# Optimization experiments

Measured on AMD Instinct MI355X. Metric: run time of the kernel, lower is better.

The kernel has to match this reference:

```python
import jax, jax.numpy as jnp
import numpy as np

N_EMBD = 1024
N_HEAD = 16

def setup_inputs() -> dict:
    key = jax.random.key(0)
    ks = jax.random.split(key, 5)
    B, T, C = 4, 2048, N_EMBD
    scale = 1.0 / np.sqrt(C)
    return {
        "x": jax.random.normal(ks[0], (B, T, C), dtype=jnp.float32),
        "w_qkv": jax.random.normal(ks[1], (C, 3 * C), dtype=jnp.float32) * scale,
        "b_qkv": jax.random.normal(ks[2], (3 * C,), dtype=jnp.float32) * 0.02,
        "w_proj": jax.random.normal(ks[3], (C, C), dtype=jnp.float32) * scale,
        "b_proj": jax.random.normal(ks[4], (C,), dtype=jnp.float32) * 0.02,
    }

def reference(x, w_qkv, b_qkv, w_proj, b_proj):
    B, T, C = x.shape
    H = N_HEAD
    D = C // H  # head dim
    qkv = x @ w_qkv + b_qkv  # [B,T,3C]
    q, k, v = jnp.split(qkv, 3, axis=-1)
    # [B,T,C] -> [B,H,T,D]
    q = q.reshape(B, T, H, D).transpose(0, 2, 1, 3)
    k = k.reshape(B, T, H, D).transpose(0, 2, 1, 3)
    v = v.reshape(B, T, H, D).transpose(0, 2, 1, 3)
    att = jnp.einsum("bhqd,bhkd->bhqk", q, k) / jnp.sqrt(jnp.asarray(D, x.dtype))
    causal = jnp.tril(jnp.ones((T, T), dtype=bool))  # [T,T]
    att = jnp.where(causal[None, None, :, :], att, -jnp.inf)
    att = jax.nn.softmax(att, axis=-1)
    y = jnp.einsum("bhqk,bhkd->bhqd", att, v)  # [B,H,T,D]
    y = y.transpose(0, 2, 1, 3).reshape(B, T, C)
    return y @ w_proj + b_proj
```

## Files before the change

### kernel.cpp

```cpp
#include <hip/hip_runtime.h>
#include <hip/hip_bf16.h>
#include <stdint.h>

typedef __bf16 bf16_8 __attribute__((ext_vector_type(8)));
typedef float f32_4 __attribute__((ext_vector_type(4)));
typedef short short4v __attribute__((ext_vector_type(4)));

static __device__ __forceinline__ unsigned short f2bf(float f) {
    union { float f; unsigned int u; } v; v.f = f;
    unsigned int u = v.u;
    unsigned int r = (u + 0x7fffu + ((u >> 16) & 1u)) >> 16;
    return (unsigned short)r;
}

static __device__ __forceinline__ unsigned int pack_bf16x2(float a, float b) {
    union { float f; unsigned int u; } ua, ub;
    ua.f = a; ub.f = b;
    return __builtin_amdgcn_perm(ub.u + 0x8000u, ua.u + 0x8000u, 0x07060302u);
}

static __device__ __forceinline__ f32_4 mfma_16x16x16_bf16(short4v a, short4v b, f32_4 c) {
#if __has_builtin(__builtin_amdgcn_mfma_f32_16x16x16bf16_1k)
    return __builtin_amdgcn_mfma_f32_16x16x16bf16_1k(a, b, c, 0, 0, 0);
#else
    asm volatile("v_mfma_f32_16x16x16_bf16 %0, %1, %2, %0"
                 : "+v"(c) : "v"(a), "v"(b));
    return c;
#endif
}

static __device__ __forceinline__ void gll16(const unsigned short* g, unsigned short* l) {
    __builtin_amdgcn_global_load_lds(
        (const __attribute__((address_space(1))) unsigned int*)g,
        (__attribute__((address_space(3))) unsigned int*)l, 16, 0, 0);
}

__global__ __launch_bounds__(256) void prep_kernel(
    const float* __restrict__ x, unsigned int* __restrict__ xbf,
    const float* __restrict__ w_qkv, unsigned short* __restrict__ wqkvt,
    const float* __restrict__ w_proj, unsigned short* __restrict__ wprojt) {
    __shared__ unsigned short tile[64][65];
    int bid = blockIdx.x;
    if (bid < 8192) {
        int i = bid * 256 + threadIdx.x;
        float4 f = ((const float4*)x)[i];
        uint2 o;
        o.x = pack_bf16x2(f.x, f.y);
        o.y = pack_bf16x2(f.z, f.w);
        ((uint2*)xbf)[i] = o;
        return;
    }
    const float* in; unsigned short* out; int N, bx, by;
    if (bid < 8960) {
        in = w_qkv; out = wqkvt; N = 3072;
        int t = bid - 8192; bx = t % 48; by = t / 48;
    } else {
        in = w_proj; out = wprojt; N = 1024;
        int t = bid - 8960; bx = t & 15; by = t >> 4;
    }
    const int K = 1024;
    int k0 = by * 64, n0 = bx * 64;
    int tc = threadIdx.x & 63, tr = threadIdx.x >> 6;
    for (int p = 0; p < 16; ++p) {
        int k = p * 4 + tr;
        tile[k][tc] = f2bf(in[(size_t)(k0 + k) * N + n0 + tc]);
    }
    __syncthreads();
    for (int p = 0; p < 16; ++p) {
        int n = p * 4 + tr;
        out[(size_t)(n0 + n) * K + k0 + tc] = tile[tc][n];
    }
}

#define BK 64
#define QSCALE 0.1803368801111204f

__global__ __launch_bounds__(256) void gemm_qkv(
    const unsigned short* __restrict__ A,
    const unsigned short* __restrict__ Bt,
    const float* __restrict__ bias,
    int M, int N, int K,
    unsigned short* __restrict__ q_out, unsigned short* __restrict__ k_out,
    unsigned short* __restrict__ v_out) {
    __shared__ __align__(16) unsigned short As[128 * BK];
    __shared__ __align__(16) unsigned short Bs[128 * BK];
    int tid = threadIdx.x;
    int wave = tid >> 6, lane = tid & 63;
    int wm = wave & 1, wn = wave >> 1;
    int quad = lane >> 4, l16 = lane & 15;
    int m0 = blockIdx.y * 128, n0 = blockIdx.x * 128;
    int which = n0 >> 10;

    f32_4 acc[4][4] = {};

    int srow = lane >> 3;
    int scs = ((lane & 7) ^ srow) * 8;
    const unsigned short* Ag = A + (size_t)(m0 + wave * 32 + srow) * K + scs;
    const unsigned short* Bg = Bt + (size_t)(n0 + wave * 32 + srow) * K + scs;
    unsigned short* Asl = As + wave * 32 * BK;
    unsigned short* Bsl = Bs + wave * 32 * BK;
    int sx = l16 & 7;

    for (int kt = 0; kt < K; kt += BK) {
        for (int p = 0; p < 4; ++p) {
            gll16(Ag + kt + (size_t)(8 * p) * K, Asl + p * 8 * BK);
            gll16(Bg + kt + (size_t)(8 * p) * K, Bsl + p * 8 * BK);
        }
        __syncthreads();
        bf16_8 af[4][2], bfr[4][2];
        for (int i = 0; i < 4; ++i)
            for (int ks = 0; ks < 2; ++ks)
                af[i][ks] = *(const bf16_8*)(As + (wm * 64 + i * 16 + l16) * BK +
                                             ((unsigned)((ks * 4 + quad) ^ sx)) * 8);
        for (int j = 0; j < 4; ++j)
            for (int ks = 0; ks < 2; ++ks)
                bfr[j][ks] = *(const bf16_8*)(Bs + (wn * 64 + j * 16 + l16) * BK +
                                              ((unsigned)((ks * 4 + quad) ^ sx)) * 8);
        if (which < 2) {
            for (int i = 0; i < 4; ++i)
                for (int j = 0; j < 4; ++j) {
                    acc[i][j] = __builtin_amdgcn_mfma_f32_16x16x32_bf16(bfr[j][0], af[i][0], acc[i][j], 0, 0, 0);
                    acc[i][j] = __builtin_amdgcn_mfma_f32_16x16x32_bf16(bfr[j][1], af[i][1], acc[i][j], 0, 0, 0);
                }
        } else {
            for (int i = 0; i < 4; ++i)
                for (int j = 0; j < 4; ++j) {
                    acc[i][j] = __builtin_amdgcn_mfma_f32_16x16x32_bf16(af[i][0], bfr[j][0], acc[i][j], 0, 0, 0);
                    acc[i][j] = __builtin_amdgcn_mfma_f32_16x16x32_bf16(af[i][1], bfr[j][1], acc[i][j], 0, 0, 0);
                }
        }
        __syncthreads();
    }

    int b = m0 >> 11;
    int tbase = (m0 & 2047) + wm * 64;
    int nw0 = n0 + wn * 64;
    if (which < 2) {
        unsigned short* dst = which == 0 ? q_out : k_out;
        float scale = which == 0 ? QSCALE : 1.0f;
        int h0 = ((n0 & 1023) >> 6) + wn;
        size_t base = ((size_t)((b << 4) + h0) * 2048) * 64;
        for (int j = 0; j < 4; ++j) {
            float4 b4 = *(const float4*)(bias + nw0 + j * 16 + quad * 4);
            int d0 = j * 16 + quad * 4;
            for (int i = 0; i < 4; ++i) {
                int t = tbase + i * 16 + l16;
                uint2 pk;
                pk.x = pack_bf16x2((acc[i][j][0] + b4.x) * scale,
                                   (acc[i][j][1] + b4.y) * scale);
                pk.y = pack_bf16x2((acc[i][j][2] + b4.z) * scale,
                                   (acc[i][j][3] + b4.w) * scale);
                *(uint2*)(dst + base + (size_t)t * 64 + d0) = pk;
            }
        }
    } else {
        for (int j = 0; j < 4; ++j) {
            int n = nw0 + j * 16 + l16;
            int c = n & 1023, h = c >> 6, d = c & 63;
            float bs = bias[n];
            size_t base = ((size_t)((b << 4) + h) * 64 + d) * 2048;
            for (int i = 0; i < 4; ++i) {
                int t0 = tbase + i * 16 + quad * 4;
                uint2 pk;
                pk.x = pack_bf16x2(acc[i][j][0] + bs, acc[i][j][1] + bs);
                pk.y = pack_bf16x2(acc[i][j][2] + bs, acc[i][j][3] + bs);
                *(uint2*)(v_out + base + t0) = pk;
            }
        }
    }
}

__global__ __launch_bounds__(256) void gemm_proj(
    const unsigned short* __restrict__ A,
    const unsigned short* __restrict__ Bt,
    const float* __restrict__ bias,
    int M, int N, int K, float* __restrict__ outf) {
    __shared__ __align__(16) unsigned short As[128 * BK];
    __shared__ __align__(16) unsigned short Bs[128 * BK];
    int tid = threadIdx.x;
    int wave = tid >> 6, lane = tid & 63;
    int wm = wave & 1, wn = wave >> 1;
    int quad = lane >> 4, l16 = lane & 15;
    int m0 = blockIdx.y * 128, n0 = blockIdx.x * 128;

    f32_4 acc[4][4] = {};

    int srow = lane >> 3;
    int scs = ((lane & 7) ^ srow) * 8;
    const unsigned short* Ag = A + (size_t)(m0 + wave * 32 + srow) * K + scs;
    const unsigned short* Bg = Bt + (size_t)(n0 + wave * 32 + srow) * K + scs;
    unsigned short* Asl = As + wave * 32 * BK;
    unsigned short* Bsl = Bs + wave * 32 * BK;
    int sx = l16 & 7;

    for (int kt = 0; kt < K; kt += BK) {
        for (int p = 0; p < 4; ++p) {
            gll16(Ag + kt + (size_t)(8 * p) * K, Asl + p * 8 * BK);
            gll16(Bg + kt + (size_t)(8 * p) * K, Bsl + p * 8 * BK);
        }
        __syncthreads();
        bf16_8 af[4][2], bfr[4][2];
        for (int i = 0; i < 4; ++i)
            for (int ks = 0; ks < 2; ++ks)
                af[i][ks] = *(const bf16_8*)(As + (wm * 64 + i * 16 + l16) * BK +
                                             ((unsigned)((ks * 4 + quad) ^ sx)) * 8);
        for (int j = 0; j < 4; ++j)
            for (int ks = 0; ks < 2; ++ks)
                bfr[j][ks] = *(const bf16_8*)(Bs + (wn * 64 + j * 16 + l16) * BK +
                                              ((unsigned)((ks * 4 + quad) ^ sx)) * 8);
        for (int i = 0; i < 4; ++i)
            for (int j = 0; j < 4; ++j) {
                acc[i][j] = __builtin_amdgcn_mfma_f32_16x16x32_bf16(af[i][0], bfr[j][0], acc[i][j], 0, 0, 0);
                acc[i][j] = __builtin_amdgcn_mfma_f32_16x16x32_bf16(af[i][1], bfr[j][1], acc[i][j], 0, 0, 0);
            }
        __syncthreads();
    }

    for (int j = 0; j < 4; ++j) {
        int n = n0 + wn * 64 + j * 16 + l16;
        float bs = bias[n];
        for (int i = 0; i < 4; ++i) {
            int m = m0 + wm * 64 + i * 16 + quad * 4;
            for (int r = 0; r < 4; ++r)
                outf[(size_t)(m + r) * N + n] = acc[i][j][r] + bs;
        }
    }
}

__global__ __launch_bounds__(256, 5) void attn_kernel(
    const unsigned short* __restrict__ Q, const unsigned short* __restrict__ Kb,
    const unsigned short* __restrict__ Vt, unsigned short* __restrict__ Y,
    int T) {
    __shared__ __align__(16) unsigned short KsB[2][64 * 64];
    __shared__ __align__(16) unsigned short VtsB[2][64 * 64];

    int tid = threadIdx.x;
    int wave = tid >> 6, lane = tid & 63;
    int quad = lane >> 4, l16 = lane & 15;
    int bh = blockIdx.x;
    int b = bh >> 4, h = bh & 15;
    int qt = 31 - blockIdx.y;
    int qw = qt * 64 + wave * 16;
    int nkt = qt + 1;

    int srow = lane >> 3;
    int scs = ((lane & 7) ^ srow) * 8;
    int sx = l16 & 7;

    bf16_8 qa[2];
    for (int ks = 0; ks < 2; ++ks)
        qa[ks] = *(const bf16_8*)(Q + ((size_t)bh * T + qw + l16) * 64 + ks * 32 + quad * 8);

    f32_4 o[4] = {};
    f32_4 osum = {};
    short4v vones;
    { unsigned short one = 0x3F80;
      vones[0] = (short)one; vones[1] = (short)one; vones[2] = (short)one; vones[3] = (short)one; }

    for (int p = 0; p < 2; ++p) {
        int row = wave * 16 + p * 8;
        gll16(Kb + ((size_t)bh * T + row + srow) * 64 + scs, &KsB[0][row * 64]);
        gll16(Vt + ((size_t)bh * 64 + row + srow) * (size_t)T + scs, &VtsB[0][row * 64]);
    }
    __syncthreads();

    for (int kt = 0; kt < nkt; ++kt) {
        int cur = kt & 1;
        int kb = kt * 64;
        if (kt + 1 < nkt) {
            int kb2 = kb + 64, nxt = cur ^ 1;
            for (int p = 0; p < 2; ++p) {
                int row = wave * 16 + p * 8;
                gll16(Kb + ((size_t)bh * T + kb2 + row + srow) * 64 + scs, &KsB[nxt][row * 64]);
                gll16(Vt + ((size_t)bh * 64 + row + srow) * (size_t)T + kb2 + scs, &VtsB[nxt][row * 64]);
            }
        }
        const unsigned short* KsC = KsB[cur];
        const unsigned short* VtsC = VtsB[cur];

        f32_4 s[4] = {};
        for (int kf = 0; kf < 4; ++kf) {
            bf16_8 k0 = *(const bf16_8*)(KsC + (kf * 16 + l16) * 64 + ((unsigned)(quad ^ sx)) * 8);
            bf16_8 k1 = *(const bf16_8*)(KsC + (kf * 16 + l16) * 64 + ((unsigned)((4 + quad) ^ sx)) * 8);
            s[kf] = __builtin_amdgcn_mfma_f32_16x16x32_bf16(k0, qa[0], s[kf], 0, 0, 0);
            s[kf] = __builtin_amdgcn_mfma_f32_16x16x32_bf16(k1, qa[1], s[kf], 0, 0, 0);
        }

        if (kt == qt) {
            int q = qw + l16;
            for (int kf = 0; kf < 4; ++kf) {
                int kk = kb + kf * 16 + quad * 4;
                for (int r = 0; r < 4; ++r)
                    if (kk + r > q) s[kf][r] = -1e30f;
            }
        }

        short4v pb[4];
        for (int kf = 0; kf < 4; ++kf) {
            float p0 = __builtin_amdgcn_exp2f(s[kf][0]);
            float p1 = __builtin_amdgcn_exp2f(s[kf][1]);
            float p2 = __builtin_amdgcn_exp2f(s[kf][2]);
            float p3 = __builtin_amdgcn_exp2f(s[kf][3]);
            union { unsigned int u[2]; short4v s4; } pu;
            pu.u[0] = pack_bf16x2(p0, p1);
            pu.u[1] = pack_bf16x2(p2, p3);
            pb[kf] = pu.s4;
        }

        for (int kf = 0; kf < 4; ++kf) {
            osum = mfma_16x16x16_bf16(vones, pb[kf], osum);
            unsigned voff = ((unsigned)((2 * kf + (quad >> 1)) ^ sx)) * 8 + (quad & 1) * 4;
            for (int df = 0; df < 4; ++df) {
                short4v va = *(const short4v*)(VtsC + (df * 16 + l16) * 64 + voff);
                o[df] = mfma_16x16x16_bf16(va, pb[kf], o[df]);
            }
        }
        __syncthreads();
    }

    float inv = 1.0f / osum[0];
    unsigned short* yp = Y + ((size_t)b * T + qw + l16) * 1024 + h * 64 + quad * 4;
    for (int df = 0; df < 4; ++df) {
        uint2 pk;
        pk.x = pack_bf16x2(o[df][0] * inv, o[df][1] * inv);
        pk.y = pack_bf16x2(o[df][2] * inv, o[df][3] * inv);
        *(uint2*)(yp + df * 16) = pk;
    }
}

extern "C" void kernel_launch(void* const* d_in, const int* in_sizes, int n_in,
                              void* d_out, int out_size, void* d_ws, size_t ws_size,
                              hipStream_t stream) {
    const float* x = (const float*)d_in[0];
    const float* w_qkv = (const float*)d_in[1];
    const float* b_qkv = (const float*)d_in[2];
    const float* w_proj = (const float*)d_in[3];
    const float* b_proj = (const float*)d_in[4];
    float* out = (float*)d_out;

    unsigned short* xbf = (unsigned short*)d_ws;
    unsigned short* wqkvt = xbf + 8388608;
    unsigned short* wprojt = wqkvt + 3145728;
    unsigned short* Qb = wprojt + 1048576;
    unsigned short* Kb = Qb + 8388608;
    unsigned short* Vtb = Kb + 8388608;
    unsigned short* Yb = Vtb + 8388608;

    hipLaunchKernelGGL(prep_kernel, dim3(9216), dim3(256), 0, stream,
                       x, (unsigned int*)xbf, w_qkv, wqkvt, w_proj, wprojt);
    hipLaunchKernelGGL(gemm_qkv, dim3(24, 64), dim3(256), 0, stream,
                       xbf, wqkvt, b_qkv, 8192, 3072, 1024,
                       Qb, Kb, Vtb);
    hipLaunchKernelGGL(attn_kernel, dim3(64, 32), dim3(256), 0, stream,
                       Qb, Kb, Vtb, Yb, 2048);
    hipLaunchKernelGGL(gemm_proj, dim3(8, 64), dim3(256), 0, stream,
                       Yb, wprojt, b_proj, 8192, 1024, 1024, out);
}
```

Measured before the change: 256.7 us.

## Restructure QKV GEMM into 256x128 tiles with triple-buffered async LDS pipeline

Measured after the change: 666.9 us. 2.6x slower.

```diff
diff --git a/kernel.cpp b/kernel.cpp
--- a/kernel.cpp
+++ b/kernel.cpp
@@ -5,6 +5,8 @@
 typedef __bf16 bf16_8 __attribute__((ext_vector_type(8)));
 typedef float f32_4 __attribute__((ext_vector_type(4)));
 typedef short short4v __attribute__((ext_vector_type(4)));
+
+#define VMCNT(n) asm volatile("s_waitcnt vmcnt(" #n ")" ::: "memory")
 
 static __device__ __forceinline__ unsigned short f2bf(float f) {
     union { float f; unsigned int u; } v; v.f = f;
@@ -75,65 +77,96 @@
 #define BK 64
 #define QSCALE 0.1803368801111204f
 
-__global__ __launch_bounds__(256) void gemm_qkv(
+__global__ __launch_bounds__(256, 2) void gemm_qkv(
     const unsigned short* __restrict__ A,
     const unsigned short* __restrict__ Bt,
     const float* __restrict__ bias,
     int M, int N, int K,
     unsigned short* __restrict__ q_out, unsigned short* __restrict__ k_out,
     unsigned short* __restrict__ v_out) {
-    __shared__ __align__(16) unsigned short As[128 * BK];
-    __shared__ __align__(16) unsigned short Bs[128 * BK];
+    __shared__ __align__(16) unsigned short Ash[3][256 * 32];
+    __shared__ __align__(16) unsigned short Bsh[3][128 * 32];
     int tid = threadIdx.x;
     int wave = tid >> 6, lane = tid & 63;
-    int wm = wave & 1, wn = wave >> 1;
     int quad = lane >> 4, l16 = lane & 15;
-    int m0 = blockIdx.y * 128, n0 = blockIdx.x * 128;
+    int wm = wave >> 1, wn = wave & 1;
+
+    int bid = blockIdx.x;
+    int flat = (bid & 7) * 96 + (bid >> 3);
+    int bm = flat / 24, bn = flat - bm * 24;
+    int m0 = bm * 256, n0 = bn * 128;
     int which = n0 >> 10;
 
-    f32_4 acc[4][4] = {};
-
-    int srow = lane >> 3;
-    int scs = ((lane & 7) ^ srow) * 8;
-    const unsigned short* Ag = A + (size_t)(m0 + wave * 32 + srow) * K + scs;
-    const unsigned short* Bg = Bt + (size_t)(n0 + wave * 32 + srow) * K + scs;
-    unsigned short* Asl = As + wave * 32 * BK;
-    unsigned short* Bsl = Bs + wave * 32 * BK;
-    int sx = l16 & 7;
-
-    for (int kt = 0; kt < K; kt += BK) {
-        for (int p = 0; p < 4; ++p) {
-            gll16(Ag + kt + (size_t)(8 * p) * K, Asl + p * 8 * BK);
-            gll16(Bg + kt + (size_t)(8 * p) * K, Bsl + p * 8 * BK);
-        }
-        __syncthreads();
-        bf16_8 af[4][2], bfr[4][2];
+    f32_4 acc[8][4] = {};
+
+    int srow = lane >> 2;
+    int gch = ((lane & 3) ^ (srow & 3)) * 8;
+    const unsigned short* Ag = A + (size_t)(m0 + wave * 16 + srow) * K + gch;
+    const unsigned short* Bg = Bt + (size_t)(n0 + wave * 16 + srow) * K + gch;
+
+    unsigned short *pa0 = Ash[0], *pa1 = Ash[1], *pa2 = Ash[2];
+    unsigned short *pb0 = Bsh[0], *pb1 = Bsh[1], *pb2 = Bsh[2];
+
+    int ktiles = K >> 5;
+    int sx8 = (quad ^ (l16 & 3)) * 8;
+
+#define STAGE_QKV(Ad, Bd, kc) do { \
+        for (int p = 0; p < 4; ++p) \
+            gll16(Ag + (kc) + (size_t)(p * 64) * K, (Ad) + (p * 64 + wave * 16) * 32); \
+        for (int p = 0; p < 2; ++p) \
+            gll16(Bg + (kc) + (size_t)(p * 64) * K, (Bd) + (p * 64 + wave * 16) * 32); \
+    } while (0)
+
+    STAGE_QKV(pa0, pb0, 0);
+    STAGE_QKV(pa1, pb1, 32);
+    VMCNT(6);
+    __builtin_amdgcn_s_barrier();
+
+    for (int kt = 0; kt < ktiles; ++kt) {
+        if (kt + 2 < ktiles) {
+            int kc = (kt + 2) << 5;
+            STAGE_QKV(pa2, pb2, kc);
+        }
+        __builtin_amdgcn_sched_barrier(0);
+
+        bf16_8 af[4], ag2[4], bfr[4];
         for (int i = 0; i < 4; ++i)
-            for (int ks = 0; ks < 2; ++ks)
-                af[i][ks] = *(const bf16_8*)(As + (wm * 64 + i * 16 + l16) * BK +
-                                             ((unsigned)((ks * 4 + quad) ^ sx)) * 8);
+            af[i] = *(const bf16_8*)(pa0 + (wm * 128 + i * 16 + l16) * 32 + sx8);
         for (int j = 0; j < 4; ++j)
-            for (int ks = 0; ks < 2; ++ks)
-                bfr[j][ks] = *(const bf16_8*)(Bs + (wn * 64 + j * 16 + l16) * BK +
-                                              ((unsigned)((ks * 4 + quad) ^ sx)) * 8);
+            bfr[j] = *(const bf16_8*)(pb0 + (wn * 64 + j * 16 + l16) * 32 + sx8);
+        for (int i = 0; i < 4; ++i)
+            ag2[i] = *(const bf16_8*)(pa0 + (wm * 128 + (i + 4) * 16 + l16) * 32 + sx8);
+
+        __builtin_amdgcn_s_setprio(1);
         if (which < 2) {
             for (int i = 0; i < 4; ++i)
-                for (int j = 0; j < 4; ++j) {
-                    acc[i][j] = __builtin_amdgcn_mfma_f32_16x16x32_bf16(bfr[j][0], af[i][0], acc[i][j], 0, 0, 0);
-                    acc[i][j] = __builtin_amdgcn_mfma_f32_16x16x32_bf16(bfr[j][1], af[i][1], acc[i][j], 0, 0, 0);
-                }
+                for (int j = 0; j < 4; ++j)
+                    acc[i][j] = __builtin_amdgcn_mfma_f32_16x16x32_bf16(bfr[j], af[i], acc[i][j], 0, 0, 0);
+            for (int i = 0; i < 4; ++i)
+                for (int j = 0; j < 4; ++j)
+                    acc[i + 4][j] = __builtin_amdgcn_mfma_f32_16x16x32_bf16(bfr[j], ag2[i], acc[i + 4][j], 0, 0, 0);
         } else {
             for (int i = 0; i < 4; ++i)
-                for (int j = 0; j < 4; ++j) {
-                    acc[i][j] = __builtin_amdgcn_mfma_f32_16x16x32_bf16(af[i][0], bfr[j][0], acc[i][j], 0, 0, 0);
-                    acc[i][j] = __builtin_amdgcn_mfma_f32_16x16x32_bf16(af[i][1], bfr[j][1], acc[i][j], 0, 0, 0);
-                }
-        }
-        __syncthreads();
-    }
+                for (int j = 0; j < 4; ++j)
+                    acc[i][j] = __builtin_amdgcn_mfma_f32_16x16x32_bf16(af[i], bfr[j], acc[i][j], 0, 0, 0);
+            for (int i = 0; i < 4; ++i)
+                for (int j = 0; j < 4; ++j)
+                    acc[i + 4][j] = __builtin_amdgcn_mfma_f32_16x16x32_bf16(ag2[i], bfr[j], acc[i + 4][j], 0, 0, 0);
+        }
+        __builtin_amdgcn_s_setprio(0);
+
+        if (kt + 1 < ktiles) {
+            if (kt + 2 < ktiles) { VMCNT(6); } else { VMCNT(0); }
+            __builtin_amdgcn_s_barrier();
+        }
+        unsigned short* t;
+        t = pa0; pa0 = pa1; pa1 = pa2; pa2 = t;
+        t = pb0; pb0 = pb1; pb1 = pb2; pb2 = t;
+    }
+#undef STAGE_QKV
 
     int b = m0 >> 11;
-    int tbase = (m0 & 2047) + wm * 64;
+    int tbase = (m0 & 2047) + wm * 128;
     int nw0 = n0 + wn * 64;
     if (which < 2) {
         unsigned short* dst = which == 0 ? q_out : k_out;
@@ -143,7 +176,7 @@
         for (int j = 0; j < 4; ++j) {
             float4 b4 = *(const float4*)(bias + nw0 + j * 16 + quad * 4);
             int d0 = j * 16 + quad * 4;
-            for (int i = 0; i < 4; ++i) {
+            for (int i = 0; i < 8; ++i) {
                 int t = tbase + i * 16 + l16;
                 uint2 pk;
                 pk.x = pack_bf16x2((acc[i][j][0] + b4.x) * scale,
@@ -159,7 +192,7 @@
             int c = n & 1023, h = c >> 6, d = c & 63;
             float bs = bias[n];
             size_t base = ((size_t)((b << 4) + h) * 64 + d) * 2048;
-            for (int i = 0; i < 4; ++i) {
+            for (int i = 0; i < 8; ++i) {
                 int t0 = tbase + i * 16 + quad * 4;
                 uint2 pk;
                 pk.x = pack_bf16x2(acc[i][j][0] + bs, acc[i][j][1] + bs);
@@ -348,7 +381,7 @@
 
     hipLaunchKernelGGL(prep_kernel, dim3(9216), dim3(256), 0, stream,
                        x, (unsigned int*)xbf, w_qkv, wqkvt, w_proj, wprojt);
-    hipLaunchKernelGGL(gemm_qkv, dim3(24, 64), dim3(256), 0, stream,
+    hipLaunchKernelGGL(gemm_qkv, dim3(768), dim3(256), 0, stream,
                        xbf, wqkvt, b_qkv, 8192, 3072, 1024,
                        Qb, Kb, Vtb);
     hipLaunchKernelGGL(attn_kernel, dim3(64, 32), dim3(256), 0, stream,
```

## Double-buffer LDS tiles in QKV and projection GEMMs to overlap loads

Applied to the files above, without the earlier changes.

Measured after the change: 254.5 us. About the same (-0.9%).

```diff
diff --git a/kernel.cpp b/kernel.cpp
--- a/kernel.cpp
+++ b/kernel.cpp
@@ -82,8 +82,8 @@
     int M, int N, int K,
     unsigned short* __restrict__ q_out, unsigned short* __restrict__ k_out,
     unsigned short* __restrict__ v_out) {
-    __shared__ __align__(16) unsigned short As[128 * BK];
-    __shared__ __align__(16) unsigned short Bs[128 * BK];
+    __shared__ __align__(16) unsigned short As[2][128 * BK];
+    __shared__ __align__(16) unsigned short Bs[2][128 * BK];
     int tid = threadIdx.x;
     int wave = tid >> 6, lane = tid & 63;
     int wm = wave & 1, wn = wave >> 1;
@@ -97,24 +97,34 @@
     int scs = ((lane & 7) ^ srow) * 8;
     const unsigned short* Ag = A + (size_t)(m0 + wave * 32 + srow) * K + scs;
     const unsigned short* Bg = Bt + (size_t)(n0 + wave * 32 + srow) * K + scs;
-    unsigned short* Asl = As + wave * 32 * BK;
-    unsigned short* Bsl = Bs + wave * 32 * BK;
+    int sbase = wave * 32 * BK;
     int sx = l16 & 7;
 
+    for (int p = 0; p < 4; ++p) {
+        gll16(Ag + (size_t)(8 * p) * K, As[0] + sbase + p * 8 * BK);
+        gll16(Bg + (size_t)(8 * p) * K, Bs[0] + sbase + p * 8 * BK);
+    }
+    __syncthreads();
+
+    int cur = 0;
     for (int kt = 0; kt < K; kt += BK) {
-        for (int p = 0; p < 4; ++p) {
-            gll16(Ag + kt + (size_t)(8 * p) * K, Asl + p * 8 * BK);
-            gll16(Bg + kt + (size_t)(8 * p) * K, Bsl + p * 8 * BK);
-        }
-        __syncthreads();
+        if (kt + BK < K) {
+            int nxt = cur ^ 1;
+            for (int p = 0; p < 4; ++p) {
+                gll16(Ag + kt + BK + (size_t)(8 * p) * K, As[nxt] + sbase + p * 8 * BK);
+                gll16(Bg + kt + BK + (size_t)(8 * p) * K, Bs[nxt] + sbase + p * 8 * BK);
+            }
+        }
+        const unsigned short* Ac = As[cur];
+        const unsigned short* Bc = Bs[cur];
         bf16_8 af[4][2], bfr[4][2];
         for (int i = 0; i < 4; ++i)
             for (int ks = 0; ks < 2; ++ks)
-                af[i][ks] = *(const bf16_8*)(As + (wm * 64 + i * 16 + l16) * BK +
+                af[i][ks] = *(const bf16_8*)(Ac + (wm * 64 + i * 16 + l16) * BK +
                                              ((unsigned)((ks * 4 + quad) ^ sx)) * 8);
         for (int j = 0; j < 4; ++j)
             for (int ks = 0; ks < 2; ++ks)
-                bfr[j][ks] = *(const bf16_8*)(Bs + (wn * 64 + j * 16 + l16) * BK +
+                bfr[j][ks] = *(const bf16_8*)(Bc + (wn * 64 + j * 16 + l16) * BK +
                                               ((unsigned)((ks * 4 + quad) ^ sx)) * 8);
         if (which < 2) {
             for (int i = 0; i < 4; ++i)
@@ -130,6 +140,7 @@
                 }
         }
         __syncthreads();
+        cur ^= 1;
     }
 
     int b = m0 >> 11;
@@ -175,8 +186,8 @@
     const unsigned short* __restrict__ Bt,
     const float* __restrict__ bias,
     int M, int N, int K, float* __restrict__ outf) {
-    __shared__ __align__(16) unsigned short As[128 * BK];
-    __shared__ __align__(16) unsigned short Bs[128 * BK];
+    __shared__ __align__(16) unsigned short As[2][128 * BK];
+    __shared__ __align__(16) unsigned short Bs[2][128 * BK];
     int tid = threadIdx.x;
     int wave = tid >> 6, lane = tid & 63;
     int wm = wave & 1, wn = wave >> 1;
@@ -189,24 +200,34 @@
     int scs = ((lane & 7) ^ srow) * 8;
     const unsigned short* Ag = A + (size_t)(m0 + wave * 32 + srow) * K + scs;
     const unsigned short* Bg = Bt + (size_t)(n0 + wave * 32 + srow) * K + scs;
-    unsigned short* Asl = As + wave * 32 * BK;
-    unsigned short* Bsl = Bs + wave * 32 * BK;
+    int sbase = wave * 32 * BK;
     int sx = l16 & 7;
 
+    for (int p = 0; p < 4; ++p) {
+        gll16(Ag + (size_t)(8 * p) * K, As[0] + sbase + p * 8 * BK);
+        gll16(Bg + (size_t)(8 * p) * K, Bs[0] + sbase + p * 8 * BK);
+    }
+    __syncthreads();
+
+    int cur = 0;
     for (int kt = 0; kt < K; kt += BK) {
-        for (int p = 0; p < 4; ++p) {
-            gll16(Ag + kt + (size_t)(8 * p) * K, Asl + p * 8 * BK);
-            gll16(Bg + kt + (size_t)(8 * p) * K, Bsl + p * 8 * BK);
-        }
-        __syncthreads();
+        if (kt + BK < K) {
+            int nxt = cur ^ 1;
+            for (int p = 0; p < 4; ++p) {
+                gll16(Ag + kt + BK + (size_t)(8 * p) * K, As[nxt] + sbase + p * 8 * BK);
+                gll16(Bg + kt + BK + (size_t)(8 * p) * K, Bs[nxt] + sbase + p * 8 * BK);
+            }
+        }
+        const unsigned short* Ac = As[cur];
+        const unsigned short* Bc = Bs[cur];
         bf16_8 af[4][2], bfr[4][2];
         for (int i = 0; i < 4; ++i)
             for (int ks = 0; ks < 2; ++ks)
-                af[i][ks] = *(const bf16_8*)(As + (wm * 64 + i * 16 + l16) * BK +
+                af[i][ks] = *(const bf16_8*)(Ac + (wm * 64 + i * 16 + l16) * BK +
                                              ((unsigned)((ks * 4 + quad) ^ sx)) * 8);
         for (int j = 0; j < 4; ++j)
             for (int ks = 0; ks < 2; ++ks)
-                bfr[j][ks] = *(const bf16_8*)(Bs + (wn * 64 + j * 16 + l16) * BK +
+                bfr[j][ks] = *(const bf16_8*)(Bc + (wn * 64 + j * 16 + l16) * BK +
                                               ((unsigned)((ks * 4 + quad) ^ sx)) * 8);
         for (int i = 0; i < 4; ++i)
             for (int j = 0; j < 4; ++j) {
@@ -214,6 +235,7 @@
                 acc[i][j] = __builtin_amdgcn_mfma_f32_16x16x32_bf16(af[i][1], bfr[j][1], acc[i][j], 0, 0, 0);
             }
         __syncthreads();
+        cur ^= 1;
     }
 
     for (int j = 0; j < 4; ++j) {
```

## Triple-buffer GEMM tiles with async prefetch and 256x128 block tiles

Applied to the files above, without the earlier changes.

After: 262.1 us. +2.1%, slower.

```diff
diff --git a/kernel.cpp b/kernel.cpp
--- a/kernel.cpp
+++ b/kernel.cpp
@@ -5,6 +5,11 @@
 typedef __bf16 bf16_8 __attribute__((ext_vector_type(8)));
 typedef float f32_4 __attribute__((ext_vector_type(4)));
 typedef short short4v __attribute__((ext_vector_type(4)));
+
+#define VMCNT(n) asm volatile("s_waitcnt vmcnt(" #n ")" ::: "memory")
+#define LGKM0 asm volatile("s_waitcnt lgkmcnt(0)" ::: "memory")
+#define SBAR __builtin_amdgcn_s_barrier()
+#define SCHB __builtin_amdgcn_sched_barrier(0)
 
 static __device__ __forceinline__ unsigned short f2bf(float f) {
     union { float f; unsigned int u; } v; v.f = f;
@@ -72,23 +77,22 @@
     }
 }
 
-#define BK 64
 #define QSCALE 0.1803368801111204f
 
-__global__ __launch_bounds__(256) void gemm_qkv(
+__global__ __launch_bounds__(512) void gemm_qkv(
     const unsigned short* __restrict__ A,
     const unsigned short* __restrict__ Bt,
     const float* __restrict__ bias,
     int M, int N, int K,
     unsigned short* __restrict__ q_out, unsigned short* __restrict__ k_out,
     unsigned short* __restrict__ v_out) {
-    __shared__ __align__(16) unsigned short As[128 * BK];
-    __shared__ __align__(16) unsigned short Bs[128 * BK];
+    __shared__ __align__(16) unsigned short As[3][256 * 64];
+    __shared__ __align__(16) unsigned short Bs[3][128 * 64];
     int tid = threadIdx.x;
     int wave = tid >> 6, lane = tid & 63;
-    int wm = wave & 1, wn = wave >> 1;
+    int wm = wave >> 1, wn = wave & 1;
     int quad = lane >> 4, l16 = lane & 15;
-    int m0 = blockIdx.y * 128, n0 = blockIdx.x * 128;
+    int m0 = blockIdx.y * 256, n0 = blockIdx.x * 128;
     int which = n0 >> 10;
 
     f32_4 acc[4][4] = {};
@@ -96,41 +100,78 @@
     int srow = lane >> 3;
     int scs = ((lane & 7) ^ srow) * 8;
     const unsigned short* Ag = A + (size_t)(m0 + wave * 32 + srow) * K + scs;
-    const unsigned short* Bg = Bt + (size_t)(n0 + wave * 32 + srow) * K + scs;
-    unsigned short* Asl = As + wave * 32 * BK;
-    unsigned short* Bsl = Bs + wave * 32 * BK;
+    const unsigned short* Bg = Bt + (size_t)(n0 + wave * 16 + srow) * K + scs;
     int sx = l16 & 7;
 
-    for (int kt = 0; kt < K; kt += BK) {
-        for (int p = 0; p < 4; ++p) {
-            gll16(Ag + kt + (size_t)(8 * p) * K, Asl + p * 8 * BK);
-            gll16(Bg + kt + (size_t)(8 * p) * K, Bsl + p * 8 * BK);
-        }
-        __syncthreads();
-        bf16_8 af[4][2], bfr[4][2];
-        for (int i = 0; i < 4; ++i)
-            for (int ks = 0; ks < 2; ++ks)
-                af[i][ks] = *(const bf16_8*)(As + (wm * 64 + i * 16 + l16) * BK +
-                                             ((unsigned)((ks * 4 + quad) ^ sx)) * 8);
+    unsigned short *a0 = As[0], *a1 = As[1], *a2 = As[2];
+    unsigned short *b0 = Bs[0], *b1 = Bs[1], *b2 = Bs[2];
+
+#define STG_A(dst, kc) do { \
+        for (int g = 0; g < 4; ++g) \
+            gll16(Ag + (kc) + (size_t)(g * 8) * K, (dst) + (wave * 32 + g * 8) * 64); \
+    } while (0)
+#define STG_B(dst, kc) do { \
+        for (int g = 0; g < 2; ++g) \
+            gll16(Bg + (kc) + (size_t)(g * 8) * K, (dst) + (wave * 16 + g * 8) * 64); \
+    } while (0)
+
+    STG_A(a0, 0); STG_B(b0, 0);
+    STG_A(a1, 64); STG_B(b1, 64);
+
+    const int nkt = K >> 6;
+    for (int kt = 0; kt < nkt; ++kt) {
+        if (kt + 1 < nkt) { VMCNT(6); } else { VMCNT(0); }
+        SCHB; SBAR; SCHB;
+        bf16_8 af[4], bfr[4];
+        for (int i = 0; i < 4; ++i)
+            af[i] = *(const bf16_8*)(a0 + (wm * 64 + i * 16 + l16) * 64 +
+                                     ((unsigned)(quad ^ sx)) * 8);
         for (int j = 0; j < 4; ++j)
-            for (int ks = 0; ks < 2; ++ks)
-                bfr[j][ks] = *(const bf16_8*)(Bs + (wn * 64 + j * 16 + l16) * BK +
-                                              ((unsigned)((ks * 4 + quad) ^ sx)) * 8);
+            bfr[j] = *(const bf16_8*)(b0 + (wn * 64 + j * 16 + l16) * 64 +
+                                      ((unsigned)(quad ^ sx)) * 8);
+        if (kt + 2 < nkt) STG_A(a2, (kt + 2) * 64);
+        SCHB; SBAR; SCHB;
+        LGKM0; SCHB;
+        __builtin_amdgcn_s_setprio(1);
         if (which < 2) {
             for (int i = 0; i < 4; ++i)
-                for (int j = 0; j < 4; ++j) {
-                    acc[i][j] = __builtin_amdgcn_mfma_f32_16x16x32_bf16(bfr[j][0], af[i][0], acc[i][j], 0, 0, 0);
-                    acc[i][j] = __builtin_amdgcn_mfma_f32_16x16x32_bf16(bfr[j][1], af[i][1], acc[i][j], 0, 0, 0);
-                }
+                for (int j = 0; j < 4; ++j)
+                    acc[i][j] = __builtin_amdgcn_mfma_f32_16x16x32_bf16(bfr[j], af[i], acc[i][j], 0, 0, 0);
         } else {
             for (int i = 0; i < 4; ++i)
-                for (int j = 0; j < 4; ++j) {
-                    acc[i][j] = __builtin_amdgcn_mfma_f32_16x16x32_bf16(af[i][0], bfr[j][0], acc[i][j], 0, 0, 0);
-                    acc[i][j] = __builtin_amdgcn_mfma_f32_16x16x32_bf16(af[i][1], bfr[j][1], acc[i][j], 0, 0, 0);
-                }
-        }
-        __syncthreads();
-    }
+                for (int j = 0; j < 4; ++j)
+                    acc[i][j] = __builtin_amdgcn_mfma_f32_16x16x32_bf16(af[i], bfr[j], acc[i][j], 0, 0, 0);
+        }
+        __builtin_amdgcn_s_setprio(0);
+
+        SCHB; SBAR; SCHB;
+        for (int i = 0; i < 4; ++i)
+            af[i] = *(const bf16_8*)(a0 + (wm * 64 + i * 16 + l16) * 64 +
+                                     ((unsigned)((4 + quad) ^ sx)) * 8);
+        for (int j = 0; j < 4; ++j)
+            bfr[j] = *(const bf16_8*)(b0 + (wn * 64 + j * 16 + l16) * 64 +
+                                      ((unsigned)((4 + quad) ^ sx)) * 8);
+        if (kt + 2 < nkt) STG_B(b2, (kt + 2) * 64);
+        SCHB; SBAR; SCHB;
+        LGKM0; SCHB;
+        __builtin_amdgcn_s_setprio(1);
+        if (which < 2) {
+            for (int i = 0; i < 4; ++i)
+                for (int j = 0; j < 4; ++j)
+                    acc[i][j] = __builtin_amdgcn_mfma_f32_16x16x32_bf16(bfr[j], af[i], acc[i][j], 0, 0, 0);
+        } else {
+            for (int i = 0; i < 4; ++i)
+                for (int j = 0; j < 4; ++j)
+                    acc[i][j] = __builtin_amdgcn_mfma_f32_16x16x32_bf16(af[i], bfr[j], acc[i][j], 0, 0, 0);
+        }
+        __builtin_amdgcn_s_setprio(0);
+
+        unsigned short* t;
+        t = a0; a0 = a1; a1 = a2; a2 = t;
+        t = b0; b0 = b1; b1 = b2; b2 = t;
+    }
+#undef STG_A
+#undef STG_B
 
     int b = m0 >> 11;
     int tbase = (m0 & 2047) + wm * 64;
@@ -170,51 +211,84 @@
     }
 }
 
-__global__ __launch_bounds__(256) void gemm_proj(
+__global__ __launch_bounds__(512) void gemm_proj(
     const unsigned short* __restrict__ A,
     const unsigned short* __restrict__ Bt,
     const float* __restrict__ bias,
     int M, int N, int K, float* __restrict__ outf) {
-    __shared__ __align__(16) unsigned short As[128 * BK];
-    __shared__ __align__(16) unsigned short Bs[128 * BK];
+    __shared__ __align__(16) unsigned short As[3][256 * 64];
+    __shared__ __align__(16) unsigned short Bs[3][128 * 64];
     int tid = threadIdx.x;
     int wave = tid >> 6, lane = tid & 63;
-    int wm = wave & 1, wn = wave >> 1;
+    int wm = wave >> 1, wn = wave & 1;
     int quad = lane >> 4, l16 = lane & 15;
-    int m0 = blockIdx.y * 128, n0 = blockIdx.x * 128;
+    int m0 = blockIdx.y * 256, n0 = blockIdx.x * 128;
 
     f32_4 acc[4][4] = {};
 
     int srow = lane >> 3;
     int scs = ((lane & 7) ^ srow) * 8;
     const unsigned short* Ag = A + (size_t)(m0 + wave * 32 + srow) * K + scs;
-    const unsigned short* Bg = Bt + (size_t)(n0 + wave * 32 + srow) * K + scs;
-    unsigned short* Asl = As + wave * 32 * BK;
-    unsigned short* Bsl = Bs + wave * 32 * BK;
+    const unsigned short* Bg = Bt + (size_t)(n0 + wave * 16 + srow) * K + scs;
     int sx = l16 & 7;
 
-    for (int kt = 0; kt < K; kt += BK) {
-        for (int p = 0; p < 4; ++p) {
-            gll16(Ag + kt + (size_t)(8 * p) * K, Asl + p * 8 * BK);
-            gll16(Bg + kt + (size_t)(8 * p) * K, Bsl + p * 8 * BK);
-        }
-        __syncthreads();
-        bf16_8 af[4][2], bfr[4][2];
-        for (int i = 0; i < 4; ++i)
-            for (int ks = 0; ks < 2; ++ks)
-                af[i][ks] = *(const bf16_8*)(As + (wm * 64 + i * 16 + l16) * BK +
-                                             ((unsigned)((ks * 4 + quad) ^ sx)) * 8);
+    unsigned short *a0 = As[0], *a1 = As[1], *a2 = As[2];
+    unsigned short *b0 = Bs[0], *b1 = Bs[1], *b2 = Bs[2];
+
+#define STG_A(dst, kc) do { \
+        for (int g = 0; g < 4; ++g) \
+            gll16(Ag + (kc) + (size_t)(g * 8) * K, (dst) + (wave * 32 + g * 8) * 64); \
+    } while (0)
+#define STG_B(dst, kc) do { \
+        for (int g = 0; g < 2; ++g) \
+            gll16(Bg + (kc) + (size_t)(g * 8) * K, (dst) + (wave * 16 + g * 8) * 64); \
+    } while (0)
+
+    STG_A(a0, 0); STG_B(b0, 0);
+    STG_A(a1, 64); STG_B(b1, 64);
+
+    const int nkt = K >> 6;
+    for (int kt = 0; kt < nkt; ++kt) {
+        if (kt + 1 < nkt) { VMCNT(6); } else { VMCNT(0); }
+        SCHB; SBAR; SCHB;
+        bf16_8 af[4], bfr[4];
+        for (int i = 0; i < 4; ++i)
+            af[i] = *(const bf16_8*)(a0 + (wm * 64 + i * 16 + l16) * 64 +
+                                     ((unsigned)(quad ^ sx)) * 8);
         for (int j = 0; j < 4; ++j)
-            for (int ks = 0; ks < 2; ++ks)
-                bfr[j][ks] = *(const bf16_8*)(Bs + (wn * 64 + j * 16 + l16) * BK +
-                                              ((unsigned)((ks * 4 + quad) ^ sx)) * 8);
-        for (int i = 0; i < 4; ++i)
-            for (int j = 0; j < 4; ++j) {
-                acc[i][j] = __builtin_amdgcn_mfma_f32_16x16x32_bf16(af[i][0], bfr[j][0], acc[i][j], 0, 0, 0);
-                acc[i][j] = __builtin_amdgcn_mfma_f32_16x16x32_bf16(af[i][1], bfr[j][1], acc[i][j], 0, 0, 0);
-            }
-        __syncthreads();
-    }
+            bfr[j] = *(const bf16_8*)(b0 + (wn * 64 + j * 16 + l16) * 64 +
+                                      ((unsigned)(quad ^ sx)) * 8);
+        if (kt + 2 < nkt) STG_A(a2, (kt + 2) * 64);
+        SCHB; SBAR; SCHB;
+        LGKM0; SCHB;
+        __builtin_amdgcn_s_setprio(1);
+        for (int i = 0; i < 4; ++i)
+            for (int j = 0; j < 4; ++j)
+                acc[i][j] = __builtin_amdgcn_mfma_f32_16x16x32_bf16(af[i], bfr[j], acc[i][j], 0, 0, 0);
+        __builtin_amdgcn_s_setprio(0);
+
+        SCHB; SBAR; SCHB;
+        for (int i = 0; i < 4; ++i)
+            af[i] = *(const bf16_8*)(a0 + (wm * 64 + i * 16 + l16) * 64 +
+                                     ((unsigned)((4 + quad) ^ sx)) * 8);
+        for (int j = 0; j < 4; ++j)
+            bfr[j] = *(const bf16_8*)(b0 + (wn * 64 + j * 16 + l16) * 64 +
+                                      ((unsigned)((4 + quad) ^ sx)) * 8);
+        if (kt + 2 < nkt) STG_B(b2, (kt + 2) * 64);
+        SCHB; SBAR; SCHB;
+        LGKM0; SCHB;
+        __builtin_amdgcn_s_setprio(1);
+        for (int i = 0; i < 4; ++i)
+            for (int j = 0; j < 4; ++j)
+                acc[i][j] = __builtin_amdgcn_mfma_f32_16x16x32_bf16(af[i], bfr[j], acc[i][j], 0, 0, 0);
+        __builtin_amdgcn_s_setprio(0);
+
+        unsigned short* t;
+        t = a0; a0 = a1; a1 = a2; a2 = t;
+        t = b0; b0 = b1; b1 = b2; b2 = t;
+    }
+#undef STG_A
+#undef STG_B
 
     for (int j = 0; j < 4; ++j) {
         int n = n0 + wn * 64 + j * 16 + l16;
@@ -348,11 +422,11 @@
 
     hipLaunchKernelGGL(prep_kernel, dim3(9216), dim3(256), 0, stream,
                        x, (unsigned int*)xbf, w_qkv, wqkvt, w_proj, wprojt);
-    hipLaunchKernelGGL(gemm_qkv, dim3(24, 64), dim3(256), 0, stream,
+    hipLaunchKernelGGL(gemm_qkv, dim3(24, 32), dim3(512), 0, stream,
                        xbf, wqkvt, b_qkv, 8192, 3072, 1024,
                        Qb, Kb, Vtb);
     hipLaunchKernelGGL(attn_kernel, dim3(64, 32), dim3(256), 0, stream,
                        Qb, Kb, Vtb, Yb, 2048);
-    hipLaunchKernelGGL(gemm_proj, dim3(8, 64), dim3(256), 0, stream,
+    hipLaunchKernelGGL(gemm_proj, dim3(8, 32), dim3(512), 0, stream,
                        Yb, wprojt, b_proj, 8192, 1024, 1024, out);
 }
```
